# Optimization experiments

Measured on AMD Instinct MI355X. Metric: run time of the kernel, lower is better.

The kernel has to match this reference:

```python
import jax, jax.numpy as jnp
import numpy as np

DIM = 512
CROSS_DIM = 512
NUM_HEADS = 8
DIM_HEAD = 64
INNER = NUM_HEADS * DIM_HEAD  # 512
SCALE = DIM_HEAD ** -0.5


def setup_inputs() -> dict:
    key = jax.random.key(0)
    ks = jax.random.split(key, 7)
    B, S, C = 2, 4096, 4096
    x = jax.random.normal(ks[0], (B, S, DIM), dtype=jnp.float32)
    context = jax.random.normal(ks[1], (B, C, CROSS_DIM), dtype=jnp.float32)
    # nn.Linear weights stored as [out, in]; we apply x @ W.T
    w_q = jax.random.normal(ks[2], (INNER, DIM), dtype=jnp.float32) * (DIM ** -0.5)
    w_k = jax.random.normal(ks[3], (INNER, CROSS_DIM), dtype=jnp.float32) * (CROSS_DIM ** -0.5)
    w_v = jax.random.normal(ks[4], (INNER, CROSS_DIM), dtype=jnp.float32) * (CROSS_DIM ** -0.5)
    w_out = jax.random.normal(ks[5], (DIM, INNER), dtype=jnp.float32) * (INNER ** -0.5)
    b_out = jax.random.normal(ks[6], (DIM,), dtype=jnp.float32) * 0.02
    return {"x": x, "context": context, "w_q": w_q, "w_k": w_k,
            "w_v": w_v, "w_out": w_out, "b_out": b_out}


def reference(x, context, w_q, w_k, w_v, w_out, b_out):
    B, S, _ = x.shape
    _, C, _ = context.shape
    # projections -> [B, H, L, Dh]
    q = (x @ w_q.T).reshape(B, S, NUM_HEADS, DIM_HEAD).transpose(0, 2, 1, 3)
    k = (context @ w_k.T).reshape(B, C, NUM_HEADS, DIM_HEAD).transpose(0, 2, 1, 3)
    v = (context @ w_v.T).reshape(B, C, NUM_HEADS, DIM_HEAD).transpose(0, 2, 1, 3)
    # scores [B, H, S, C]
    scores = jnp.einsum('bhsd,bhcd->bhsc', q, k) * SCALE
    attn = jax.nn.softmax(scores, axis=-1)
    out = jnp.einsum('bhsc,bhcd->bhsd', attn, v)  # [B,H,S,Dh]
    out = out.transpose(0, 2, 1, 3).reshape(B, S, INNER)
    return out @ w_out.T + b_out
```

## Files before the change

### kernel.cpp

```cpp
#include <hip/hip_runtime.h>

typedef __bf16 bf16;
typedef __bf16 bf16x2 __attribute__((ext_vector_type(2)));
typedef __bf16 bf16x4 __attribute__((ext_vector_type(4)));
typedef __bf16 bf16x8 __attribute__((ext_vector_type(8)));
typedef float  f32x4  __attribute__((ext_vector_type(4)));
typedef float  f32x16 __attribute__((ext_vector_type(16)));
typedef unsigned int uint4v __attribute__((ext_vector_type(4)));

#define MFMA16(a,b,c) __builtin_amdgcn_mfma_f32_16x16x32_bf16(a,b,c,0,0,0)
#define MFMA32(a,b,c) __builtin_amdgcn_mfma_f32_32x32x16_bf16(a,b,c,0,0,0)

#if __has_builtin(__builtin_amdgcn_exp2f)
#define EXP2(x) __builtin_amdgcn_exp2f(x)
#else
#define EXP2(x) exp2f(x)
#endif

__device__ __forceinline__ void gl16(const bf16* __restrict__ g, bf16* l)
{
#if __has_builtin(__builtin_amdgcn_global_load_lds)
    __builtin_amdgcn_global_load_lds(
        (const __attribute__((address_space(1))) void*)g,
        (__attribute__((address_space(3))) void*)l, 16, 0, 0);
#else
    const int ln = __builtin_amdgcn_mbcnt_hi(~0u, __builtin_amdgcn_mbcnt_lo(~0u, 0));
    *(bf16x8*)((bf16*)l + ln * 8) = *(const bf16x8*)g;
#endif
}

__device__ __forceinline__ bf16x8 ld8_f32_to_bf16(const float* __restrict__ p)
{
    f32x4 a = *(const f32x4*)p;
    f32x4 b = *(const f32x4*)(p + 4);
    bf16x8 o;
#pragma unroll
    for (int j = 0; j < 4; j++) { o[j] = (bf16)a[j]; o[4 + j] = (bf16)b[j]; }
    return o;
}

__device__ __forceinline__ float max3f(float a, float b, float c)
{
    return fmaxf(fmaxf(a, b), c);
}

__device__ __forceinline__ float rmax16(const f32x16& s)
{
    const float a0 = max3f(s[0],  s[1],  s[2]);
    const float a1 = max3f(s[3],  s[4],  s[5]);
    const float a2 = max3f(s[6],  s[7],  s[8]);
    const float a3 = max3f(s[9],  s[10], s[11]);
    const float a4 = max3f(s[12], s[13], s[14]);
    return fmaxf(max3f(a0, a1, a2), max3f(a3, a4, s[15]));
}

__global__ __launch_bounds__(256) void cvt6(
    const float* __restrict__ x,  const float* __restrict__ ctx,
    const float* __restrict__ wq, const float* __restrict__ wk,
    const float* __restrict__ wv, const float* __restrict__ wout,
    bf16* __restrict__ xb, bf16* __restrict__ cb, bf16* __restrict__ wqb,
    bf16* __restrict__ wkb, bf16* __restrict__ wvb, bf16* __restrict__ wob)
{
    const int bid = blockIdx.x;
    const float* s; bf16* d; int base;
    if      (bid < 2048) { s = x;    d = xb;  base = 0;    }
    else if (bid < 4096) { s = ctx;  d = cb;  base = 2048; }
    else if (bid < 4224) { s = wq;   d = wqb; base = 4096; }
    else if (bid < 4352) { s = wk;   d = wkb; base = 4224; }
    else if (bid < 4480) { s = wv;   d = wvb; base = 4352; }
    else                 { s = wout; d = wob; base = 4480; }
    const int i = ((bid - base) * 256 + threadIdx.x) * 8;
    *(bf16x8*)&d[i] = ld8_f32_to_bf16(s + i);
}

__global__ __launch_bounds__(256, 3) void mm_qkv(
    const bf16* __restrict__ xb, const bf16* __restrict__ cb,
    const bf16* __restrict__ wqb, const bf16* __restrict__ wkb,
    const bf16* __restrict__ wvb,
    bf16* __restrict__ Qb, bf16* __restrict__ Kb, bf16* __restrict__ Vtb)
{
    __shared__ bf16 Al[128 * 32];
    __shared__ bf16 Wl[128 * 32];

    const int L  = blockIdx.x + 4 * (blockIdx.y + 64 * blockIdx.z);
    const int L2 = (L & 7) * 96 + (L >> 3);
    const int bx = L2 & 3;
    const int by = (L2 >> 2) & 63;
    const int z  = L2 >> 8;

    const bf16* A; const bf16* W; bf16* out; int mode;
    if (z == 0)      { A = xb; W = wqb; out = Qb;  mode = 0; }
    else if (z == 1) { A = cb; W = wkb; out = Kb;  mode = 0; }
    else             { A = cb; W = wvb; out = Vtb; mode = 1; }

    const int tid  = threadIdx.x;
    const int lane = tid & 63;
    const int w    = tid >> 6;
    const int wr   = w >> 1, wc = w & 1;
    const int q    = lane >> 4, m0 = lane & 15;

    f32x4 acc[4][4];
#pragma unroll
    for (int i = 0; i < 4; i++)
#pragma unroll
        for (int j = 0; j < 4; j++)
#pragma unroll
            for (int r = 0; r < 4; r++) acc[i][j][r] = 0.f;

    const bf16* Ab = A + (size_t)(by * 128) * 512;
    const bf16* Wb = W + (size_t)(bx * 128) * 512;
    const int sr = w * 16 + (lane >> 2);
    const int sc = (lane & 3) * 8;

    for (int k0 = 0; k0 < 512; k0 += 32) {
        gl16(Ab + (size_t)sr * 512 + k0 + sc,        &Al[(w * 16) * 32]);
        gl16(Ab + (size_t)(sr + 64) * 512 + k0 + sc, &Al[(64 + w * 16) * 32]);
        gl16(Wb + (size_t)sr * 512 + k0 + sc,        &Wl[(w * 16) * 32]);
        gl16(Wb + (size_t)(sr + 64) * 512 + k0 + sc, &Wl[(64 + w * 16) * 32]);
        __syncthreads();

        bf16x8 af[4], wf[4];
#pragma unroll
        for (int mt = 0; mt < 4; mt++)
            af[mt] = *(const bf16x8*)&Al[(wr * 64 + mt * 16 + m0) * 32 + q * 8];
#pragma unroll
        for (int nt = 0; nt < 4; nt++)
            wf[nt] = *(const bf16x8*)&Wl[(wc * 64 + nt * 16 + m0) * 32 + q * 8];
#pragma unroll
        for (int mt = 0; mt < 4; mt++)
#pragma unroll
            for (int nt = 0; nt < 4; nt++)
                acc[mt][nt] = MFMA16(af[mt], wf[nt], acc[mt][nt]);
        __syncthreads();
    }

#pragma unroll
    for (int nt = 0; nt < 4; nt++) {
        const int col = bx * 128 + wc * 64 + nt * 16 + m0;
#pragma unroll
        for (int mt = 0; mt < 4; mt++) {
            const int row0 = by * 128 + wr * 64 + mt * 16 + q * 4;
            if (mode == 0) {
#pragma unroll
                for (int r = 0; r < 4; r++)
                    out[(size_t)(row0 + r) * 512 + col] = (bf16)acc[mt][nt][r];
            } else {
                const int bb = row0 >> 12, c = row0 & 4095;
                const int hh = col >> 6,  d = col & 63;
                bf16x4 o4;
#pragma unroll
                for (int r = 0; r < 4; r++) o4[r] = (bf16)acc[mt][nt][r];
                *(bf16x4*)&out[(size_t)((bb * 8 + hh) * 64 + d) * 4096 + c] = o4;
            }
        }
    }
}

__global__ __launch_bounds__(256, 4) void mm_oproj(
    const bf16* __restrict__ Ob, const bf16* __restrict__ wob,
    const float* __restrict__ bout, float* __restrict__ out)
{
    __shared__ bf16 Al[64 * 32];
    __shared__ bf16 Wl[64 * 32];

    const int L  = blockIdx.x + 8 * blockIdx.y;
    const int L2 = (L & 7) * 128 + (L >> 3);
    const int bx = L2 & 7;
    const int by = L2 >> 3;

    const int tid  = threadIdx.x;
    const int lane = tid & 63;
    const int w    = tid >> 6;
    const int wr   = w >> 1, wc = w & 1;
    const int q    = lane >> 4, m0 = lane & 15;

    f32x4 acc[2][2];
#pragma unroll
    for (int i = 0; i < 2; i++)
#pragma unroll
        for (int j = 0; j < 2; j++)
#pragma unroll
            for (int r = 0; r < 4; r++) acc[i][j][r] = 0.f;

    const bf16* Ab = Ob  + (size_t)(by * 64) * 512;
    const bf16* Wb = wob + (size_t)(bx * 64) * 512;
    const int sr = w * 16 + (lane >> 2);
    const int sc = (lane & 3) * 8;

    for (int k0 = 0; k0 < 512; k0 += 32) {
        gl16(Ab + (size_t)sr * 512 + k0 + sc, &Al[(w * 16) * 32]);
        gl16(Wb + (size_t)sr * 512 + k0 + sc, &Wl[(w * 16) * 32]);
        __syncthreads();

        bf16x8 af[2], wf[2];
#pragma unroll
        for (int mt = 0; mt < 2; mt++)
            af[mt] = *(const bf16x8*)&Al[(wr * 32 + mt * 16 + m0) * 32 + q * 8];
#pragma unroll
        for (int nt = 0; nt < 2; nt++)
            wf[nt] = *(const bf16x8*)&Wl[(wc * 32 + nt * 16 + m0) * 32 + q * 8];
#pragma unroll
        for (int mt = 0; mt < 2; mt++)
#pragma unroll
            for (int nt = 0; nt < 2; nt++)
                acc[mt][nt] = MFMA16(af[mt], wf[nt], acc[mt][nt]);
        __syncthreads();
    }

#pragma unroll
    for (int nt = 0; nt < 2; nt++) {
        const int col = bx * 64 + wc * 32 + nt * 16 + m0;
        const float bv = bout[col];
#pragma unroll
        for (int mt = 0; mt < 2; mt++) {
#pragma unroll
            for (int r = 0; r < 4; r++) {
                const int row = by * 64 + wr * 32 + mt * 16 + q * 4 + r;
                out[(size_t)row * 512 + col] = acc[mt][nt][r] + bv;
            }
        }
    }
}

__global__ __launch_bounds__(256, 2) void fa_attn(
    const bf16* __restrict__ Qb, const bf16* __restrict__ Kb,
    const bf16* __restrict__ Vtb, bf16* __restrict__ Ob,
    float* __restrict__ Opart, float2* __restrict__ ml, const int nsplit)
{
    __shared__ bf16 Kl[2][64 * 72];
    __shared__ bf16 Vl[2][64 * 72];

    const int tid  = threadIdx.x;
    const int lane = tid & 63;
    const int w    = tid >> 6;
    const int n0   = lane & 31;
    const int hd   = lane >> 5;

    const int nper = 64 * nsplit;
    const int L  = blockIdx.x + 32 * (blockIdx.y + 8 * blockIdx.z);
    const int L2 = (L & 7) * nper + (L >> 3);
    const int qx = L2 & 31;
    const int yz = L2 >> 5;
    const int h0 = yz & 7;
    const int zz = yz >> 3;
    const int b  = (nsplit == 2) ? (zz >> 1) : zz;
    const int ch = (nsplit == 2) ? (zz & 1) : 0;
    const int clen = (nsplit == 2) ? 2048 : 4096;
    const int c0 = ch * clen;
    const int qg = qx * 128 + w * 32;

    const float qsc = 0.125f * 1.44269504089f;
    bf16x8 qf[4];
    const bf16* qp = Qb + (size_t)(b * 4096 + qg + n0) * 512 + h0 * 64 + hd * 8;
#pragma unroll
    for (int ks = 0; ks < 4; ks++) {
        bf16x8 t = *(const bf16x8*)(qp + ks * 16);
#pragma unroll
        for (int j = 0; j < 8; j++) t[j] = (bf16)((float)t[j] * qsc);
        qf[ks] = t;
    }

    f32x16 oc[2];
#pragma unroll
    for (int dt = 0; dt < 2; dt++)
#pragma unroll
        for (int r = 0; r < 16; r++) oc[dt][r] = 0.f;
    float mrun = 0.f, lrun = 0.f;

    const int srow = tid >> 2;
    const int scol = (tid & 3) * 16;
    const bf16* Kg = Kb  + (size_t)(b * 4096) * 512 + h0 * 64;
    const bf16* Vg = Vtb + (size_t)(b * 8 + h0) * 64 * 4096;

#define STAGE(buf, cb_) do { \
    *(bf16x8*)&Kl[buf][srow * 72 + scol]     = *(const bf16x8*)(Kg + (size_t)((cb_) + srow) * 512 + scol); \
    *(bf16x8*)&Kl[buf][srow * 72 + scol + 8] = *(const bf16x8*)(Kg + (size_t)((cb_) + srow) * 512 + scol + 8); \
    *(bf16x8*)&Vl[buf][srow * 72 + scol]     = *(const bf16x8*)(Vg + (size_t)srow * 4096 + (cb_) + scol); \
    *(bf16x8*)&Vl[buf][srow * 72 + scol + 8] = *(const bf16x8*)(Vg + (size_t)srow * 4096 + (cb_) + scol + 8); \
} while (0)

    STAGE(0, c0);
    int cur = 0;

    for (int cb = c0; cb < c0 + clen; cb += 64) {
        __syncthreads();
        if (cb + 64 < c0 + clen) STAGE(cur ^ 1, cb + 64);

        const bf16* Kc = &Kl[cur][0];
        const bf16* Vc = &Vl[cur][0];

        f32x16 st[2];
        __builtin_amdgcn_s_setprio(1);
#pragma unroll
        for (int ct = 0; ct < 2; ct++) {
#pragma unroll
            for (int r = 0; r < 16; r++) st[ct][r] = -mrun;
#pragma unroll
            for (int ks = 0; ks < 4; ks++) {
                bf16x8 kf = *(const bf16x8*)&Kc[(ct * 32 + n0) * 72 + ks * 16 + hd * 8];
                st[ct] = MFMA32(kf, qf[ks], st[ct]);
            }
        }
        __builtin_amdgcn_s_setprio(0);

        float mx = fmaxf(rmax16(st[0]), rmax16(st[1]));
        mx = fmaxf(mx, __shfl_xor(mx, 32));

        if (__any(mx > 8.f)) {
            const float d  = fmaxf(mx, 0.f);
            const float al = EXP2(-d);
            mrun += d;
            lrun *= al;
#pragma unroll
            for (int dt = 0; dt < 2; dt++)
#pragma unroll
                for (int r = 0; r < 16; r++) oc[dt][r] *= al;
#pragma unroll
            for (int ct = 0; ct < 2; ct++)
#pragma unroll
                for (int r = 0; r < 16; r++) st[ct][r] -= d;
        }

        unsigned int pd[2][4][2];
        float rs4[4];
#pragma unroll
        for (int g = 0; g < 4; g++) rs4[g] = 0.f;
#pragma unroll
        for (int ct = 0; ct < 2; ct++)
#pragma unroll
            for (int g = 0; g < 4; g++)
#pragma unroll
                for (int t = 0; t < 2; t++) {
                    const float e0 = EXP2(st[ct][4 * g + 2 * t]);
                    const float e1 = EXP2(st[ct][4 * g + 2 * t + 1]);
                    rs4[g] += e0 + e1;
                    bf16x2 pr; pr[0] = (bf16)e0; pr[1] = (bf16)e1;
                    pd[ct][g][t] = __builtin_bit_cast(unsigned int, pr);
                }
        float rs = (rs4[0] + rs4[1]) + (rs4[2] + rs4[3]);
        rs += __shfl_xor(rs, 32);
        lrun += rs;

        __builtin_amdgcn_s_setprio(1);
#pragma unroll
        for (int ks = 0; ks < 4; ks++) {
            const int ct = ks >> 1;
            const int g0 = 2 * (ks & 1), g1 = g0 + 1;
            const unsigned int own0  = hd ? pd[ct][g1][0] : pd[ct][g0][0];
            const unsigned int own1  = hd ? pd[ct][g1][1] : pd[ct][g0][1];
            const unsigned int send0 = hd ? pd[ct][g0][0] : pd[ct][g1][0];
            const unsigned int send1 = hd ? pd[ct][g0][1] : pd[ct][g1][1];
            const unsigned int r0 = (unsigned int)__shfl_xor((int)send0, 32);
            const unsigned int r1 = (unsigned int)__shfl_xor((int)send1, 32);
            uint4v u;
            u[0] = hd ? r0 : own0;
            u[1] = hd ? r1 : own1;
            u[2] = hd ? own0 : r0;
            u[3] = hd ? own1 : r1;
            const bf16x8 pf = __builtin_bit_cast(bf16x8, u);
#pragma unroll
            for (int dt = 0; dt < 2; dt++) {
                bf16x8 vf = *(const bf16x8*)&Vc[(dt * 32 + n0) * 72 + ks * 16 + hd * 8];
                oc[dt] = MFMA32(vf, pf, oc[dt]);
            }
        }
        __builtin_amdgcn_s_setprio(0);
        cur ^= 1;
    }
#undef STAGE

    if (nsplit == 1) {
        const float rli = 1.0f / lrun;
        bf16* ob = Ob + (size_t)(b * 4096 + qg + n0) * 512 + h0 * 64;
#pragma unroll
        for (int dt = 0; dt < 2; dt++)
#pragma unroll
            for (int rq = 0; rq < 4; rq++) {
                bf16x4 o4;
#pragma unroll
                for (int i = 0; i < 4; i++) o4[i] = (bf16)(oc[dt][4 * rq + i] * rli);
                *(bf16x4*)&ob[dt * 32 + rq * 8 + hd * 4] = o4;
            }
    } else {
        float* Op = Opart + ((size_t)(ch * 2 + b) * 4096 + qg + n0) * 512 + h0 * 64;
#pragma unroll
        for (int dt = 0; dt < 2; dt++)
#pragma unroll
            for (int rq = 0; rq < 4; rq++) {
                f32x4 o4;
#pragma unroll
                for (int i = 0; i < 4; i++) o4[i] = oc[dt][4 * rq + i];
                *(f32x4*)&Op[dt * 32 + rq * 8 + hd * 4] = o4;
            }
        if (hd == 0)
            ml[((size_t)(ch * 2 + b) * 8 + h0) * 4096 + qg + n0] = make_float2(mrun, lrun);
    }
}

__global__ __launch_bounds__(256) void fa_merge(
    const float* __restrict__ Opart, const float2* __restrict__ ml,
    bf16* __restrict__ Ob)
{
    const int e   = blockIdx.x * 256 + threadIdx.x;
    const int row = e >> 7;
    const int c4  = (e & 127) * 4;
    const int b   = row >> 12, sr = row & 4095, h = c4 >> 6;

    const float2 u = ml[((size_t)(0 + b) * 8 + h) * 4096 + sr];
    const float2 v = ml[((size_t)(2 + b) * 8 + h) * 4096 + sr];
    const float m  = fmaxf(u.x, v.x);
    const float w1 = EXP2(u.x - m), w2 = EXP2(v.x - m);
    const float rL = 1.0f / (u.y * w1 + v.y * w2);

    const f32x4 o1 = *(const f32x4*)&Opart[((size_t)(0 + b) * 4096 + sr) * 512 + c4];
    const f32x4 o2 = *(const f32x4*)&Opart[((size_t)(2 + b) * 4096 + sr) * 512 + c4];
    bf16x4 o;
#pragma unroll
    for (int i = 0; i < 4; i++) o[i] = (bf16)((o1[i] * w1 + o2[i] * w2) * rL);
    *(bf16x4*)&Ob[(size_t)row * 512 + c4] = o;
}

__global__ void ws_sig11(float* out) { if (threadIdx.x == 0) out[0] = 777.0f; }

extern "C" void kernel_launch(void* const* d_in, const int* in_sizes, int n_in,
                              void* d_out, int out_size, void* d_ws, size_t ws_size,
                              hipStream_t stream)
{
    const float* x    = (const float*)d_in[0];
    const float* ctx  = (const float*)d_in[1];
    const float* wq   = (const float*)d_in[2];
    const float* wk   = (const float*)d_in[3];
    const float* wv   = (const float*)d_in[4];
    const float* wout = (const float*)d_in[5];
    const float* bout = (const float*)d_in[6];
    float* out = (float*)d_out;

    char* ws = (char*)d_ws;
    const size_t MB = 1024 * 1024;
    const size_t SZ = (size_t)8192 * 512 * sizeof(bf16);
    if (ws_size < 66 * MB) {
        ws_sig11<<<dim3(1), dim3(64), 0, stream>>>(out);
        return;
    }

    bf16* Qb  = (bf16*)(ws);
    bf16* Kb  = (bf16*)(ws + SZ);
    bf16* Vtb = (bf16*)(ws + 2 * SZ);
    bf16* Ob  = (bf16*)(ws + 3 * SZ);

    bf16* xb  = (bf16*)(ws + 32 * MB);
    bf16* cbf = (bf16*)(ws + 40 * MB);
    bf16* wqb = (bf16*)(ws + 48 * MB);
    bf16* wkb = (bf16*)(ws + 48 * MB + 512 * 1024);
    bf16* wvb = (bf16*)(ws + 49 * MB);
    float*  Opart = (float*)(ws + 32 * MB);
    float2* mlp   = (float2*)(ws + 64 * MB);
    bf16*   wob   = (bf16*)(ws + 65 * MB);

    cvt6    <<<dim3(4608), dim3(256), 0, stream>>>(x, ctx, wq, wk, wv, wout,
                                                   xb, cbf, wqb, wkb, wvb, wob);
    mm_qkv  <<<dim3(4, 64, 3), dim3(256), 0, stream>>>(xb, cbf, wqb, wkb, wvb, Qb, Kb, Vtb);
    fa_attn <<<dim3(32, 8, 4), dim3(256), 0, stream>>>(Qb, Kb, Vtb, Ob, Opart, mlp, 2);
    fa_merge<<<dim3(4096), dim3(256), 0, stream>>>(Opart, mlp, Ob);
    mm_oproj<<<dim3(8, 128), dim3(256), 0, stream>>>(Ob, wob, bout, out);
}
```

Baseline: 214.0 us.

## Stage K/V via direct global-to-LDS loads with XOR swizzle; speculate softmax rescale

```diff
diff --git a/kernel.cpp b/kernel.cpp
--- a/kernel.cpp
+++ b/kernel.cpp
@@ -227,8 +227,8 @@
     const bf16* __restrict__ Vtb, bf16* __restrict__ Ob,
     float* __restrict__ Opart, float2* __restrict__ ml, const int nsplit)
 {
-    __shared__ bf16 Kl[2][64 * 72];
-    __shared__ bf16 Vl[2][64 * 72];
+    __shared__ bf16 Kl[2][64 * 64];
+    __shared__ bf16 Vl[2][64 * 64];
 
     const int tid  = threadIdx.x;
     const int lane = tid & 63;
@@ -267,16 +267,17 @@
         for (int r = 0; r < 16; r++) oc[dt][r] = 0.f;
     float mrun = 0.f, lrun = 0.f;
 
-    const int srow = tid >> 2;
-    const int scol = (tid & 3) * 16;
+    const int lr  = lane >> 3;
+    const int g8  = ((lane & 7) ^ lr) * 8;
     const bf16* Kg = Kb  + (size_t)(b * 4096) * 512 + h0 * 64;
     const bf16* Vg = Vtb + (size_t)(b * 8 + h0) * 64 * 4096;
+    const int swz = n0 & 7;
 
 #define STAGE(buf, cb_) do { \
-    *(bf16x8*)&Kl[buf][srow * 72 + scol]     = *(const bf16x8*)(Kg + (size_t)((cb_) + srow) * 512 + scol); \
-    *(bf16x8*)&Kl[buf][srow * 72 + scol + 8] = *(const bf16x8*)(Kg + (size_t)((cb_) + srow) * 512 + scol + 8); \
-    *(bf16x8*)&Vl[buf][srow * 72 + scol]     = *(const bf16x8*)(Vg + (size_t)srow * 4096 + (cb_) + scol); \
-    *(bf16x8*)&Vl[buf][srow * 72 + scol + 8] = *(const bf16x8*)(Vg + (size_t)srow * 4096 + (cb_) + scol + 8); \
+    gl16(Kg + (size_t)((cb_) + w * 16 + lr) * 512 + g8,      &Kl[buf][(w * 16) * 64]); \
+    gl16(Kg + (size_t)((cb_) + w * 16 + 8 + lr) * 512 + g8,  &Kl[buf][(w * 16 + 8) * 64]); \
+    gl16(Vg + (size_t)(w * 16 + lr) * 4096 + (cb_) + g8,     &Vl[buf][(w * 16) * 64]); \
+    gl16(Vg + (size_t)(w * 16 + 8 + lr) * 4096 + (cb_) + g8, &Vl[buf][(w * 16 + 8) * 64]); \
 } while (0)
 
     STAGE(0, c0);
@@ -297,7 +298,7 @@
             for (int r = 0; r < 16; r++) st[ct][r] = -mrun;
 #pragma unroll
             for (int ks = 0; ks < 4; ks++) {
-                bf16x8 kf = *(const bf16x8*)&Kc[(ct * 32 + n0) * 72 + ks * 16 + hd * 8];
+                bf16x8 kf = *(const bf16x8*)&Kc[(ct * 32 + n0) * 64 + ((2 * ks + hd) ^ swz) * 8];
                 st[ct] = MFMA32(kf, qf[ks], st[ct]);
             }
         }
@@ -305,21 +306,6 @@
 
         float mx = fmaxf(rmax16(st[0]), rmax16(st[1]));
         mx = fmaxf(mx, __shfl_xor(mx, 32));
-
-        if (__any(mx > 8.f)) {
-            const float d  = fmaxf(mx, 0.f);
-            const float al = EXP2(-d);
-            mrun += d;
-            lrun *= al;
-#pragma unroll
-            for (int dt = 0; dt < 2; dt++)
-#pragma unroll
-                for (int r = 0; r < 16; r++) oc[dt][r] *= al;
-#pragma unroll
-            for (int ct = 0; ct < 2; ct++)
-#pragma unroll
-                for (int r = 0; r < 16; r++) st[ct][r] -= d;
-        }
 
         unsigned int pd[2][4][2];
         float rs4[4];
@@ -338,6 +324,32 @@
                     pd[ct][g][t] = __builtin_bit_cast(unsigned int, pr);
                 }
         float rs = (rs4[0] + rs4[1]) + (rs4[2] + rs4[3]);
+
+        if (__builtin_expect(__any(mx > 8.f), 0)) {
+            const float d  = fmaxf(mx, 0.f);
+            const float al = EXP2(-d);
+            mrun += d;
+            lrun *= al;
+#pragma unroll
+            for (int dt = 0; dt < 2; dt++)
+#pragma unroll
+                for (int r = 0; r < 16; r++) oc[dt][r] *= al;
+#pragma unroll
+            for (int g = 0; g < 4; g++) rs4[g] = 0.f;
+#pragma unroll
+            for (int ct = 0; ct < 2; ct++)
+#pragma unroll
+                for (int g = 0; g < 4; g++)
+#pragma unroll
+                    for (int t = 0; t < 2; t++) {
+                        const float e0 = EXP2(st[ct][4 * g + 2 * t]     - d);
+                        const float e1 = EXP2(st[ct][4 * g + 2 * t + 1] - d);
+                        rs4[g] += e0 + e1;
+                        bf16x2 pr; pr[0] = (bf16)e0; pr[1] = (bf16)e1;
+                        pd[ct][g][t] = __builtin_bit_cast(unsigned int, pr);
+                    }
+            rs = (rs4[0] + rs4[1]) + (rs4[2] + rs4[3]);
+        }
         rs += __shfl_xor(rs, 32);
         lrun += rs;
 
@@ -360,7 +372,7 @@
             const bf16x8 pf = __builtin_bit_cast(bf16x8, u);
 #pragma unroll
             for (int dt = 0; dt < 2; dt++) {
-                bf16x8 vf = *(const bf16x8*)&Vc[(dt * 32 + n0) * 72 + ks * 16 + hd * 8];
+                bf16x8 vf = *(const bf16x8*)&Vc[(dt * 32 + n0) * 64 + ((2 * ks + hd) ^ swz) * 8];
                 oc[dt] = MFMA32(vf, pf, oc[dt]);
             }
         }
```

Result: slower. 233.2 us (+9.0%).
